# Kernel optimization log

Measured on AMD Instinct MI355X. Metric: run time of the kernel, lower is better.

The kernel has to match this reference:

```python
import jax, jax.numpy as jnp
import numpy as np

IMG = 224
RADIUS_CUTS, AZIMUTH_CUTS = 16, 64
N_RADIUS, N_AZIMUTH = 25, 16          # kr1*kr2 = 25, ka^2 = 16
N_R = RADIUS_CUTS * N_RADIUS          # 400 sampled radii
N_A = AZIMUTH_CUTS * N_AZIMUTH        # 1024 sampled azimuths
EMBED_DIM = 96
KR, KA = 5, 4


def sample_grid(dist, H, W):
    """Per-batch polar sampling coordinates for the spherical distortion model.
    dist: (B, 4) polynomial distortion coefficients (module does dist.transpose(1,0)).
    Returns grid (B, N_R, N_A, 2) in grid_sample convention (x=width coord first),
    and theta_max (B,).
    """
    B = dist.shape[0]
    cf = 0.2 + dist.T                      # (4, B), positive odd-poly coefficients
    c = cf[:, :, None]                     # (4, B, 1) for broadcasting
    theta_max = jnp.full((B,), jnp.pi / 2, dtype=dist.dtype)

    def poly(t):                           # odd polynomial r(theta), t: (B, n)
        t2 = t * t
        return t * (c[0] + t2 * (c[1] + t2 * (c[2] + t2 * c[3])))

    # midpoint theta samples in (0, theta_max)
    theta = theta_max[:, None] * (jnp.arange(N_R, dtype=dist.dtype) + 0.5) / N_R  # (B, N_R)
    r = poly(theta) / poly(theta_max[:, None]) * (H * 0.5)                        # (B, N_R) pixels from center

    phi = (2.0 * jnp.pi) * (jnp.arange(N_A, dtype=dist.dtype) + 0.5) / N_A        # (N_A,)
    xc = r[:, :, None] * jnp.cos(phi)      # (B, N_R, N_A)
    yc = r[:, :, None] * jnp.sin(phi)
    # module: out = cat((yc/(W//2), xc/(H//2)), dim=3)
    grid = jnp.stack([yc / (W // 2), xc / (H // 2)], axis=-1)
    return grid, theta_max


def grid_sample_bilinear(img, grid):
    """torch.nn.functional.grid_sample, bilinear, align_corners=True, zeros padding.
    img: (B,C,H,W), grid: (B,Ho,Wo,2) with grid[...,0]=x (width), grid[...,1]=y (height).
    """
    B, C, H, W = img.shape
    gx = (grid[..., 0] + 1.0) * 0.5 * (W - 1)   # align_corners=True mapping
    gy = (grid[..., 1] + 1.0) * 0.5 * (H - 1)
    x0 = jnp.floor(gx); y0 = jnp.floor(gy)
    wx1 = gx - x0; wx0 = 1.0 - wx1
    wy1 = gy - y0; wy0 = 1.0 - wy1

    def corner(xi, yi, w):
        valid = (xi >= 0) & (xi <= W - 1) & (yi >= 0) & (yi <= H - 1)
        xc_ = jnp.clip(xi, 0, W - 1).astype(jnp.int32)
        yc_ = jnp.clip(yi, 0, H - 1).astype(jnp.int32)
        v = jax.vmap(lambda im, yy, xx: im[:, yy, xx])(img, yc_, xc_)  # (B,C,Ho,Wo)
        return v * (w * valid)[:, None, :, :]

    return (corner(x0, y0, wx0 * wy0) + corner(x0 + 1, y0, wx1 * wy0)
            + corner(x0, y0 + 1, wx0 * wy1) + corner(x0 + 1, y0 + 1, wx1 * wy1))


def conv2d(x, w, b, stride):
    y = jax.lax.conv_general_dilated(x, w, window_strides=stride, padding='VALID',
                                     dimension_numbers=('NCHW', 'OIHW', 'NCHW'))
    return y + b[None, :, None, None]


def setup_inputs() -> dict:
    key = jax.random.key(0)
    k = jax.random.split(key, 6)
    x = jax.random.uniform(k[0], (32, 3, IMG, IMG), dtype=jnp.float32)
    dist = jax.random.uniform(k[1], (32, 4), dtype=jnp.float32)
    w1 = jax.random.normal(k[2], (EMBED_DIM, 3, KR, KA), dtype=jnp.float32) * 0.05
    b1 = jnp.zeros((EMBED_DIM,), dtype=jnp.float32)
    w2 = jax.random.normal(k[3], (EMBED_DIM, EMBED_DIM, KR, KA), dtype=jnp.float32) * 0.05
    b2 = jnp.zeros((EMBED_DIM,), dtype=jnp.float32)
    return {"x": x, "dist": dist, "w1": w1, "b1": b1, "w2": w2, "b2": b2}


def reference(x, dist, w1, b1, w2, b2):
    B, C, H, W = x.shape
    grid, theta_max = sample_grid(dist, H, W)          # (B,400,1024,2)
    sampled = grid_sample_bilinear(x, grid)            # (B,3,400,1024)
    t = conv2d(sampled, w1, b1, (KR, KA))              # (B,96,80,256)
    t = conv2d(t, w2, b2, (KR, KA))                    # (B,96,16,64)
    t = t.reshape(B, EMBED_DIM, -1).transpose(0, 2, 1) # (B,1024,96)
    return (t, theta_max)
```

## Files before the change

### kernel.cpp

```cpp
#include <hip/hip_runtime.h>
#include <hip/hip_bf16.h>
#include <math.h>

#define NBATCH 32
#define IMGSZ  224
#define NR     400
#define NA     1024
#define ED     96
#define SROW   266

typedef __attribute__((ext_vector_type(8))) __bf16 bf16x8;
typedef __attribute__((ext_vector_type(8), aligned(8))) __bf16 bf16x8u;
typedef __attribute__((ext_vector_type(4), aligned(8))) __bf16 bf16x4a;
typedef __attribute__((ext_vector_type(4))) __bf16 bf16x4;
typedef __attribute__((ext_vector_type(4))) float f32x4;

union frag_u { struct { bf16x4a lo, hi; } p; bf16x8 v; };


#define PACK_N   (NBATCH*IMGSZ*IMGSZ)
#define PACK_B   ((PACK_N + 255)/256)
#define PREP_N   (ED*ED*20 + 12*64*8 + NBATCH*NR + NA + NBATCH)
#define PREP_B   ((PREP_N + 255)/256)

__global__ __launch_bounds__(256)
void prep_pack_kernel(const float* __restrict__ x,
                      const float* __restrict__ dist,
                      const float* __restrict__ w1,
                      const float* __restrict__ w2,
                      __bf16* __restrict__ xp,
                      float* __restrict__ rtab,
                      float* __restrict__ costab,
                      float* __restrict__ sintab,
                      __bf16* __restrict__ w2f,
                      __bf16* __restrict__ w1f,
                      float* __restrict__ theta_out) {
    const float PI = 3.14159265358979323846f;
    const float SC = 223.0f / 224.0f;
    int bid = blockIdx.x;

    if (bid < PACK_B) {
        int idx = bid*256 + threadIdx.x;
        if (idx >= PACK_N) return;
        int b  = idx / (IMGSZ*IMGSZ);
        int px = idx - b*(IMGSZ*IMGSZ);
        const float* p = x + (size_t)b*3*IMGSZ*IMGSZ + px;
        bf16x4 o;
        o[0] = (__bf16)p[0];
        o[1] = (__bf16)p[IMGSZ*IMGSZ];
        o[2] = (__bf16)p[2*IMGSZ*IMGSZ];
        o[3] = (__bf16)0.0f;
        *(bf16x4*)(xp + (size_t)idx*4) = o;
        return;
    }

    int idx = (bid - PACK_B)*256 + threadIdx.x;
    if (idx < ED*ED*20) {
        int j    = idx & 7;
        int lane = (idx >> 3) & 63;
        int grp  = idx >> 9;
        int nt   = grp % 6;
        int t    = grp / 6;
        int icb  = t % 3;
        int p    = t / 3;
        int sw   = (((p & 3) + icb) & 1) * 4;
        int oc = nt*16 + (lane & 15);
        int ic = icb*32 + (lane >> 4)*8 + (j ^ sw);
        w2f[idx] = (__bf16)w2[((size_t)(oc*ED + ic)*5 + (p >> 2))*4 + (p & 3)];
    } else if (idx < ED*ED*20 + 12*64*8) {
        int i2   = idx - ED*ED*20;
        int j    = i2 & 7;
        int lane = (i2 >> 3) & 63;
        int grp  = i2 >> 9;
        int ks = grp / 6, ot = grp % 6;
        int oc = ot*16 + (lane & 15);
        int k  = ks*32 + (lane >> 4)*8 + j;
        w1f[i2] = (k < 60) ? (__bf16)w1[oc*60 + k] : (__bf16)0.0f;
    } else if (idx < ED*ED*20 + 12*64*8 + NBATCH*NR) {
        int i2 = idx - ED*ED*20 - 12*64*8;
        int b = i2 / NR, i = i2 % NR;
        float c0 = 0.2f + dist[b*4+0];
        float c1 = 0.2f + dist[b*4+1];
        float c2 = 0.2f + dist[b*4+2];
        float c3 = 0.2f + dist[b*4+3];
        float tmax = 0.5f * PI;
        float t  = tmax * ((float)i + 0.5f) / (float)NR;
        float t2 = t * t;
        float pt = t * (c0 + t2*(c1 + t2*(c2 + t2*c3)));
        float tm2 = tmax * tmax;
        float pm = tmax * (c0 + tm2*(c1 + tm2*(c2 + tm2*c3)));
        rtab[i2] = pt / pm * (0.5f * (float)IMGSZ);
    } else if (idx < ED*ED*20 + 12*64*8 + NBATCH*NR + NA) {
        int j = idx - ED*ED*20 - 12*64*8 - NBATCH*NR;
        float phi = 2.0f * PI * ((float)j + 0.5f) / (float)NA;
        costab[j] = cosf(phi) * SC;
        sintab[j] = sinf(phi) * SC;
    } else if (idx < PREP_N) {
        theta_out[idx - (ED*ED*20 + 12*64*8 + NBATCH*NR + NA)] = 0.5f * PI;
    }
}

__global__ __launch_bounds__(256, 4)
void mega_kernel(const __bf16* __restrict__ xp,
                 const __bf16* __restrict__ w1f_g,
                 const __bf16* __restrict__ w2f,
                 const float* __restrict__ b1,
                 const float* __restrict__ b2,
                 const float* __restrict__ rtab,
                 const float* __restrict__ costab,
                 const float* __restrict__ sintab,
                 float* __restrict__ out) {
    __shared__ __attribute__((aligned(16))) char smem[32576];
    __bf16* s_samp = (__bf16*)smem;
    __bf16* t1f    = (__bf16*)(smem + 8000);
    __bf16* s_w1f  = (__bf16*)(smem + 20288);
    float*  red    = (float*)smem;

    int tid = threadIdx.x;
    int bid = blockIdx.x;
    int r2 = bid & 15;
    int aq = (bid >> 4) & 3;
    int b  = bid >> 6;
    int wave = tid >> 6, lane = tid & 63, l15 = lane & 15, quad = lane >> 4;

    #pragma unroll
    for (int i = 0; i < 3; ++i)
        *(bf16x8*)(s_w1f + i*2048 + tid*8) = *(const bf16x8*)(w1f_g + i*2048 + tid*8);

    int az = aq*256 + tid;
    float sn = sintab[az];
    float cs = costab[az];
    const __bf16* xpb = xp + (size_t)b*IMGSZ*IMGSZ*4;
    const float* rb = rtab + b*NR + r2*25;

    f32x4 acc2[6];
    #pragma unroll
    for (int nt = 0; nt < 6; ++nt) acc2[nt] = (f32x4){0.f,0.f,0.f,0.f};

    auto sample = [&](int kr) {
        #pragma unroll
        for (int q = 0; q < 5; ++q) {
            float r  = rb[kr*5 + q];
            float gx = fmaf(r, sn, 111.5f);
            float gy = fmaf(r, cs, 111.5f);
            float x0f = floorf(gx), y0f = floorf(gy);
            float wx1 = gx - x0f, wx0 = 1.0f - wx1;
            float wy1 = gy - y0f, wy0 = 1.0f - wy1;
            int ix = (int)x0f, iy = (int)y0f;
            ix = min(max(ix, 0), IMGSZ-2);
            iy = min(max(iy, 0), IMGSZ-2);
            const __bf16* img = xpb + ((size_t)iy*IMGSZ + ix)*4;
            bf16x8u p0 = *(const bf16x8u*)img;
            bf16x8u p1 = *(const bf16x8u*)(img + IMGSZ*4);
            float w00 = wy0*wx0, w01 = wy0*wx1, w10 = wy1*wx0, w11 = wy1*wx1;
            #pragma unroll
            for (int c = 0; c < 3; ++c) {
                float v = w00*(float)p0[c] + w01*(float)p0[4+c]
                        + w10*(float)p1[c] + w11*(float)p1[4+c];
                s_samp[(c*5 + q)*SROW + tid] = (__bf16)v;
            }
        }
    };

    sample(0);

    for (int kr = 0; kr < 5; ++kr) {
        __syncthreads();

        int colb = (wave*16 + l15)*4;
        f32x4 acc1[6];
        #pragma unroll
        for (int ot = 0; ot < 6; ++ot) acc1[ot] = (f32x4){0.f,0.f,0.f,0.f};

        frag_u fa, fb;
        fa.p.lo = *(const bf16x4a*)&s_samp[(quad*2    )*SROW + colb];
        fa.p.hi = *(const bf16x4a*)&s_samp[(quad*2 + 1)*SROW + colb];
        fb.p.lo = *(const bf16x4a*)&s_samp[(8 + quad*2)*SROW + colb];
        if (quad == 3) fb.p.hi = (bf16x4a){};
        else           fb.p.hi = *(const bf16x4a*)&s_samp[(9 + quad*2)*SROW + colb];

        #pragma unroll
        for (int ot = 0; ot < 6; ++ot) {
            bf16x8 wf0 = *(const bf16x8*)(s_w1f + (ot     )*512 + lane*8);
            bf16x8 wf1 = *(const bf16x8*)(s_w1f + (6 + ot )*512 + lane*8);
            acc1[ot] = __builtin_amdgcn_mfma_f32_16x16x32_bf16(wf0, fa.v, acc1[ot], 0, 0, 0);
            acc1[ot] = __builtin_amdgcn_mfma_f32_16x16x32_bf16(wf1, fb.v, acc1[ot], 0, 0, 0);
        }

        int pixel = wave*16 + l15;
        int a2l = pixel >> 2, ka = pixel & 3;
        #pragma unroll
        for (int ot = 0; ot < 6; ++ot) {
            f32x4 v = acc1[ot] + *(const f32x4*)(b1 + ot*16 + quad*4);
            bf16x4a wv;
            wv[0] = (__bf16)v[0]; wv[1] = (__bf16)v[1];
            wv[2] = (__bf16)v[2]; wv[3] = (__bf16)v[3];
            int icbase = ot*16 + quad*4;
            int kk = ka*3 + (icbase >> 5);
            int qT = (icbase >> 3) & 3;
            int jb = (icbase & 7) ^ ((kk & 1)*4);
            *(bf16x4a*)&t1f[((kk*4 + qT)*16 + a2l)*8 + jb] = wv;
        }
        __syncthreads();

        #pragma unroll
        for (int icb = 0; icb < 3; ++icb) {
            int kk = wave*3 + icb;
            int p  = kr*4 + wave;
            bf16x8 af = *(const bf16x8*)&t1f[(kk*64 + lane)*8];
            const __bf16* wp = w2f + (size_t)((p*3 + icb)*6)*512 + lane*8;
            #pragma unroll
            for (int nt = 0; nt < 6; ++nt) {
                bf16x8 bf = *(const bf16x8*)(wp + nt*512);
                acc2[nt] = __builtin_amdgcn_mfma_f32_16x16x32_bf16(af, bf, acc2[nt], 0, 0, 0);
            }
        }

        __builtin_amdgcn_sched_barrier(0);

        if (kr < 4) sample(kr + 1);
    }

    __syncthreads();
    if (wave) {
        float* rw = red + (wave - 1)*1568;
        #pragma unroll
        for (int nt = 0; nt < 6; ++nt)
            #pragma unroll
            for (int r = 0; r < 4; ++r)
                rw[(quad*4 + r)*98 + nt*16 + l15] = acc2[nt][r];
    }
    __syncthreads();
    if (wave == 0) {
        size_t ob = ((size_t)b*1024 + r2*64 + aq*16)*ED;
        #pragma unroll
        for (int nt = 0; nt < 6; ++nt) {
            int oc = nt*16 + l15;
            float bias = b2[oc];
            #pragma unroll
            for (int r = 0; r < 4; ++r) {
                int row = quad*4 + r;
                float v = acc2[nt][r] + bias
                        + red[row*98 + oc]
                        + red[1568 + row*98 + oc]
                        + red[3136 + row*98 + oc];
                out[ob + (size_t)row*ED + oc] = v;
            }
        }
    }
}

extern "C" void kernel_launch(void* const* d_in, const int* in_sizes, int n_in,
                              void* d_out, int out_size, void* d_ws, size_t ws_size,
                              hipStream_t stream) {
    const float* x    = (const float*)d_in[0];
    const float* dist = (const float*)d_in[1];
    const float* w1   = (const float*)d_in[2];
    const float* b1   = (const float*)d_in[3];
    const float* w2   = (const float*)d_in[4];
    const float* b2   = (const float*)d_in[5];
    float* out = (float*)d_out;

    float* rtab   = (float*)d_ws;
    float* costab = rtab + NBATCH*NR;
    float* sintab = costab + NA;
    __bf16* w2f   = (__bf16*)(sintab + NA);
    __bf16* w1f   = w2f + ED*ED*20;
    __bf16* xp    = w1f + 12*64*8;

    float* theta_out = out + (size_t)NBATCH*1024*ED;

    prep_pack_kernel<<<PACK_B + PREP_B, 256, 0, stream>>>(
        x, dist, w1, w2, xp, rtab, costab, sintab, w2f, w1f, theta_out);
    mega_kernel<<<NBATCH*16*4, 256, 0, stream>>>(
        xp, w1f, w2f, b1, b2, rtab, costab, sintab, out);
}
```

Baseline: 140.4 us.

## Read conv1 weights from global, shrink LDS, raise occupancy, vectorize input pack

The fused kernel stops staging the conv1 weight fragments in shared memory and loads them straight from global (L1/L2-cached) memory inside the MFMA loop. This cuts the LDS footprint from about 32.5KB to about 20KB and raises the launch-bounds occupancy hint from 4 to 8 blocks per CU, aiming for more latency hiding. Separately, the input pack kernel now handles four pixels per thread using 16-byte float4 loads and bf16x8 stores. The trade-off is repeated global weight loads in the inner loop, plus possible register pressure or spills from the tighter occupancy target.

```diff
diff --git a/kernel.cpp b/kernel.cpp
--- a/kernel.cpp
+++ b/kernel.cpp
@@ -19,7 +19,8 @@
 
 
 #define PACK_N   (NBATCH*IMGSZ*IMGSZ)
-#define PACK_B   ((PACK_N + 255)/256)
+#define PACK_N4  (PACK_N/4)
+#define PACK_B   ((PACK_N4 + 255)/256)
 #define PREP_N   (ED*ED*20 + 12*64*8 + NBATCH*NR + NA + NBATCH)
 #define PREP_B   ((PREP_N + 255)/256)
 
@@ -40,17 +41,22 @@
     int bid = blockIdx.x;
 
     if (bid < PACK_B) {
-        int idx = bid*256 + threadIdx.x;
-        if (idx >= PACK_N) return;
+        int i4 = bid*256 + threadIdx.x;
+        if (i4 >= PACK_N4) return;
+        int idx = i4 * 4;
         int b  = idx / (IMGSZ*IMGSZ);
         int px = idx - b*(IMGSZ*IMGSZ);
         const float* p = x + (size_t)b*3*IMGSZ*IMGSZ + px;
-        bf16x4 o;
-        o[0] = (__bf16)p[0];
-        o[1] = (__bf16)p[IMGSZ*IMGSZ];
-        o[2] = (__bf16)p[2*IMGSZ*IMGSZ];
-        o[3] = (__bf16)0.0f;
-        *(bf16x4*)(xp + (size_t)idx*4) = o;
+        f32x4 cr = *(const f32x4*)(p);
+        f32x4 cg = *(const f32x4*)(p + IMGSZ*IMGSZ);
+        f32x4 cb = *(const f32x4*)(p + 2*IMGSZ*IMGSZ);
+        bf16x8 o0, o1;
+        o0[0] = (__bf16)cr[0]; o0[1] = (__bf16)cg[0]; o0[2] = (__bf16)cb[0]; o0[3] = (__bf16)0.0f;
+        o0[4] = (__bf16)cr[1]; o0[5] = (__bf16)cg[1]; o0[6] = (__bf16)cb[1]; o0[7] = (__bf16)0.0f;
+        o1[0] = (__bf16)cr[2]; o1[1] = (__bf16)cg[2]; o1[2] = (__bf16)cb[2]; o1[3] = (__bf16)0.0f;
+        o1[4] = (__bf16)cr[3]; o1[5] = (__bf16)cg[3]; o1[6] = (__bf16)cb[3]; o1[7] = (__bf16)0.0f;
+        *(bf16x8*)(xp + (size_t)idx*4)     = o0;
+        *(bf16x8*)(xp + (size_t)idx*4 + 8) = o1;
         return;
     }
 
@@ -100,7 +106,7 @@
     }
 }
 
-__global__ __launch_bounds__(256, 4)
+__global__ __launch_bounds__(256, 8)
 void mega_kernel(const __bf16* __restrict__ xp,
                  const __bf16* __restrict__ w1f_g,
                  const __bf16* __restrict__ w2f,
@@ -110,10 +116,9 @@
                  const float* __restrict__ costab,
                  const float* __restrict__ sintab,
                  float* __restrict__ out) {
-    __shared__ __attribute__((aligned(16))) char smem[32576];
+    __shared__ __attribute__((aligned(16))) char smem[20288];
     __bf16* s_samp = (__bf16*)smem;
     __bf16* t1f    = (__bf16*)(smem + 8000);
-    __bf16* s_w1f  = (__bf16*)(smem + 20288);
     float*  red    = (float*)smem;
 
     int tid = threadIdx.x;
@@ -122,10 +127,6 @@
     int aq = (bid >> 4) & 3;
     int b  = bid >> 6;
     int wave = tid >> 6, lane = tid & 63, l15 = lane & 15, quad = lane >> 4;
-
-    #pragma unroll
-    for (int i = 0; i < 3; ++i)
-        *(bf16x8*)(s_w1f + i*2048 + tid*8) = *(const bf16x8*)(w1f_g + i*2048 + tid*8);
 
     int az = aq*256 + tid;
     float sn = sintab[az];
@@ -181,8 +182,8 @@
 
         #pragma unroll
         for (int ot = 0; ot < 6; ++ot) {
-            bf16x8 wf0 = *(const bf16x8*)(s_w1f + (ot     )*512 + lane*8);
-            bf16x8 wf1 = *(const bf16x8*)(s_w1f + (6 + ot )*512 + lane*8);
+            bf16x8 wf0 = *(const bf16x8*)(w1f_g + (ot     )*512 + lane*8);
+            bf16x8 wf1 = *(const bf16x8*)(w1f_g + (6 + ot )*512 + lane*8);
             acc1[ot] = __builtin_amdgcn_mfma_f32_16x16x32_bf16(wf0, fa.v, acc1[ot], 0, 0, 0);
             acc1[ot] = __builtin_amdgcn_mfma_f32_16x16x32_bf16(wf1, fb.v, acc1[ot], 0, 0, 0);
         }
```

Result: slower. 264.6 us (+88.5%).
